# Kernel tuning notes

Hardware: AMD Instinct MI355X
Metric: run time of the kernel (lower is better)

## Reference

```python
import jax, jax.numpy as jnp
import numpy as np

N_NODES = 10000
N_REL = 50
R_AUG = 2 * N_REL + 1  # forward + inverse + self-loop relation
D_EMB = 128
D_H1 = 128
D_H2 = 128
N_EDGES = 320000
N_BATCH = 65536


def setup_inputs() -> dict:
    key = jax.random.key(0)
    ks = jax.random.split(key, 10)
    s = jax.random.randint(ks[0], (N_EDGES,), 0, N_NODES)
    p = jax.random.randint(ks[1], (N_EDGES,), 0, N_REL)
    o = jax.random.randint(ks[2], (N_EDGES,), 0, N_NODES)
    graph = jnp.stack([s, p, o], axis=1)  # [E,3] (subject, relation, object)
    bs = jax.random.randint(ks[3], (N_BATCH,), 0, N_NODES)
    bp = jax.random.randint(ks[4], (N_BATCH,), 0, N_REL)
    bo = jax.random.randint(ks[5], (N_BATCH,), 0, N_NODES)
    batch = jnp.stack([bs, bp, bo], axis=1)  # [B,3] triples to score
    node_embeddings = jax.random.normal(ks[6], (N_NODES, D_EMB), jnp.float32) * 0.02
    W1 = jax.random.normal(ks[7], (R_AUG, D_EMB, D_H1), jnp.float32) * 0.02
    b1 = jnp.zeros((D_H1,), jnp.float32)
    W2 = jax.random.normal(ks[8], (R_AUG, D_H1, D_H2), jnp.float32) * 0.02
    b2 = jnp.zeros((D_H2,), jnp.float32)
    relations = jax.random.normal(ks[9], (N_REL, D_H2), jnp.float32) * 0.02
    return {"graph": graph, "batch": batch, "node_embeddings": node_embeddings,
            "W1": W1, "b1": b1, "W2": W2, "b2": b2, "relations": relations}


def _augment_edges(graph):
    # Add inverse relations (r + N_REL) and self-loops (relation 2*N_REL),
    # matching torch-rgcn's num_relations = nrel*2 + 1 construction.
    s, p, o = graph[:, 0], graph[:, 1], graph[:, 2]
    loop = jnp.arange(N_NODES, dtype=graph.dtype)
    src = jnp.concatenate([s, o, loop])
    rel = jnp.concatenate([p, p + N_REL, jnp.full((N_NODES,), 2 * N_REL, graph.dtype)])
    dst = jnp.concatenate([o, s, loop])
    return src, rel, dst


def _rgcn_layer(x, src, rel, dst, W, b):
    # Per-(relation, target-node) row normalization 1/c_{i,r}, then
    # h_i = sum_r W_r^T * sum_{j in N_r(i)} x_j / c_{i,r} + b
    seg = rel * N_NODES + dst  # segment id over stacked (R*N) adjacency rows
    deg = jax.ops.segment_sum(jnp.ones_like(seg, dtype=x.dtype), seg,
                              num_segments=R_AUG * N_NODES)
    norm = 1.0 / jnp.maximum(deg, 1.0)
    msg = x[src] * norm[seg][:, None]                      # [Etot, d_in]
    agg = jax.ops.segment_sum(msg, seg, num_segments=R_AUG * N_NODES)
    agg = agg.reshape(R_AUG, N_NODES, -1)                  # [R, N, d_in]
    return jnp.einsum('rnd,rdo->no', agg, W) + b           # [N, d_out]


def reference(graph, batch, node_embeddings, W1, b1, W2, b2, relations):
    src, rel, dst = _augment_edges(graph)
    x = _rgcn_layer(node_embeddings, src, rel, dst, W1, b1)
    x = jax.nn.relu(x)
    x = _rgcn_layer(x, src, rel, dst, W2, b2)
    # DistMult scoring: gather s/p/o embeddings, elementwise multiply, reduce.
    s_e = x[batch[:, 0]]
    p_e = relations[batch[:, 1]]
    o_e = x[batch[:, 2]]
    return (s_e * p_e * o_e).sum(axis=1)  # [B]
```

## Files before the change

### kernel.cpp

```cpp
#include <hip/hip_runtime.h>

#define N_NODES 10000
#define N_RELS  50
#define R_AUG   101
#define D       128
#define N_EDGES 320000
#define E_AUG   650000
#define N_BATCH 65536

#define NBINS   N_NODES
#define NSB     ((NBINS + 255) / 256)
#define NP      (R_AUG * N_NODES)
#define NPB4    ((NP + 1023) / 1024)
#define BSPAN   512
#define GEMM_NBLK (101 + (E_AUG + BSPAN - 1) / BSPAN)
#define SCAT_BLOCKS ((E_AUG + 255) / 256)

#define HIST_BLOCKS  2540
#define TW_BLOCKS    808
#define PREPX_BLOCKS 1250

typedef short bf16x8 __attribute__((ext_vector_type(8)));
typedef float f32x4  __attribute__((ext_vector_type(4)));

__device__ __forceinline__ unsigned short f2bf(float f) {
    union { float f; unsigned int u; } v; v.f = f;
    unsigned int r = (v.u + 0x7FFFu + ((v.u >> 16) & 1u)) >> 16;
    return (unsigned short)r;
}
__device__ __forceinline__ float bf2f(unsigned short h) {
    union { unsigned int u; float f; } v; v.u = ((unsigned int)h) << 16;
    return v.f;
}
__device__ __forceinline__ float u2f(unsigned int u) {
    union { unsigned int u; float f; } v; v.u = u; return v.f;
}
__device__ __forceinline__ unsigned int f2u(float f) {
    union { float f; unsigned int u; } v; v.f = f; return v.u;
}

__device__ __forceinline__ void decode_edge(const int* __restrict__ g, int e,
                                            int& src, int& rel, int& dst) {
    if (e < N_EDGES)            { src = g[3*e];     rel = g[3*e+1];          dst = g[3*e+2]; }
    else if (e < 2*N_EDGES)     { int b = e - N_EDGES;
                                  src = g[3*b+2];   rel = g[3*b+1] + N_RELS; dst = g[3*b];   }
    else                        { int n = e - 2*N_EDGES; src = n; dst = n; rel = 2*N_RELS;   }
}

__device__ __forceinline__ int pair_rel(int r) {
    return (r < N_RELS) ? r + N_RELS : (r < 2 * N_RELS ? r - N_RELS : r);
}


__global__ __launch_bounds__(256) void prep_all(const float* __restrict__ x,
                                                unsigned short* __restrict__ xb,
                                                const float* __restrict__ W1,
                                                const float* __restrict__ W2,
                                                unsigned short* __restrict__ W1t,
                                                unsigned short* __restrict__ W2t,
                                                const int* __restrict__ g,
                                                int* __restrict__ deg) {
    __shared__ float tile[64][65];
    int b = blockIdx.x, t = threadIdx.x;
    if (b < HIST_BLOCKS) {
        int e = b * 256 + t;
        if (e < E_AUG) {
            int src, rel, dst;
            decode_edge(g, e, src, rel, dst);
            atomicAdd(&deg[rel * N_NODES + dst], 1);
        }
    } else if (b < HIST_BLOCKS + TW_BLOCKS) {
        int q = b - HIST_BLOCKS;
        int d0 = (q & 1) * 64, o0 = ((q >> 1) & 1) * 64;
        int z = q >> 2;
        const float* W = (z < R_AUG) ? W1 : W2;
        unsigned short* Wt = (z < R_AUG) ? W1t : W2t;
        int r = (z < R_AUG) ? z : (z - R_AUG);
        int tx = t & 63, ty = t >> 6;
        #pragma unroll
        for (int i = ty; i < 64; i += 4)
            tile[i][tx] = W[((size_t)r * D + (d0 + i)) * D + (o0 + tx)];
        __syncthreads();
        #pragma unroll
        for (int i = ty; i < 64; i += 4)
            Wt[((size_t)r * D + (o0 + i)) * D + (d0 + tx)] = f2bf(tile[tx][i]);
    } else {
        int i = (b - HIST_BLOCKS - TW_BLOCKS) * 1024 + t * 4;
        float4 xv = *(const float4*)(x + i);
        ushort4 o;
        o.x = f2bf(xv.x); o.y = f2bf(xv.y); o.z = f2bf(xv.z); o.w = f2bf(xv.w);
        *(ushort4*)(xb + i) = o;
    }
}


__global__ __launch_bounds__(256) void scan_a(const int* __restrict__ deg,
                                              int* __restrict__ offs,
                                              int* __restrict__ part,
                                              int* __restrict__ S,
                                              int* __restrict__ ppart) {
    __shared__ int wsum[4];
    int t = threadIdx.x, lane = t & 63, w = t >> 6;
    int b = blockIdx.x;
    if (b < NSB) {
        int i = b * 256 + t;
        int v = 0;
        if (i < NBINS) {
            for (int r = 0; r < R_AUG; r++) v += deg[r * N_NODES + i];
        }
        int incl = v;
        #pragma unroll
        for (int off = 1; off < 64; off <<= 1) {
            int u = __shfl_up(incl, off, 64);
            if (lane >= off) incl += u;
        }
        if (lane == 63) wsum[w] = incl;
        __syncthreads();
        int woff = 0;
        for (int k = 0; k < w; k++) woff += wsum[k];
        if (i < NBINS) offs[i] = woff + incl - v;
        if (t == 255) part[b] = woff + incl;
    } else {
        int pb = b - NSB;
        int i0 = pb * 1024 + t * 4;
        int4 f = {0, 0, 0, 0};
        if (i0 < NP) {
            int r = i0 / N_NODES;
            int xx = i0 - r * N_NODES;
            const int* dp = deg + pair_rel(r) * N_NODES + xx;
            if (i0 + 3 < NP) {
                int4 d = *(const int4*)dp;
                f.x = d.x > 0; f.y = d.y > 0; f.z = d.z > 0; f.w = d.w > 0;
            } else {
                f.x = dp[0] > 0;
                if (i0 + 1 < NP) f.y = dp[1] > 0;
                if (i0 + 2 < NP) f.z = dp[2] > 0;
            }
        }
        int e1 = f.x, e2 = f.x + f.y, e3 = e2 + f.z, v = e3 + f.w;
        int incl = v;
        #pragma unroll
        for (int off = 1; off < 64; off <<= 1) {
            int u = __shfl_up(incl, off, 64);
            if (lane >= off) incl += u;
        }
        if (lane == 63) wsum[w] = incl;
        __syncthreads();
        int woff = 0;
        for (int k = 0; k < w; k++) woff += wsum[k];
        int texcl = woff + incl - v;
        if (i0 + 3 < NP) {
            int4 o = {texcl, texcl + e1, texcl + e2, texcl + e3};
            *(int4*)(S + i0) = o;
        } else if (i0 < NP) {
            S[i0] = texcl;
            if (i0 + 1 < NP) S[i0 + 1] = texcl + e1;
            if (i0 + 2 < NP) S[i0 + 2] = texcl + e2;
        }
        if (t == 255) ppart[pb] = woff + incl;
    }
}


__global__ __launch_bounds__(256) void scan_b(int* __restrict__ part,
                                              int* __restrict__ ppart,
                                              int* __restrict__ S) {
    __shared__ int wsum[4];
    int t = threadIdx.x, lane = t & 63, w = t >> 6;
    if (blockIdx.x == 0) {
        int v = (t < NSB) ? part[t] : 0;
        int incl = v;
        #pragma unroll
        for (int off = 1; off < 64; off <<= 1) {
            int u = __shfl_up(incl, off, 64);
            if (lane >= off) incl += u;
        }
        if (lane == 63) wsum[w] = incl;
        __syncthreads();
        int woff = 0;
        for (int k = 0; k < w; k++) woff += wsum[k];
        if (t < NSB) part[t] = woff + incl - v;
    } else {
        int carry = 0;
        for (int base = 0; base < NPB4; base += 256) {
            int i = base + t;
            int v = (i < NPB4) ? ppart[i] : 0;
            int incl = v;
            #pragma unroll
            for (int off = 1; off < 64; off <<= 1) {
                int u = __shfl_up(incl, off, 64);
                if (lane >= off) incl += u;
            }
            if (lane == 63) wsum[w] = incl;
            __syncthreads();
            int woff = 0;
            for (int k = 0; k < w; k++) woff += wsum[k];
            if (i < NPB4) ppart[i] = carry + woff + incl - v;
            carry += wsum[0] + wsum[1] + wsum[2] + wsum[3];
            __syncthreads();
        }
        if (t == 0) S[NP] = carry;
    }
}


__global__ __launch_bounds__(256) void scan_c(int* __restrict__ offs,
                                              const int* __restrict__ part,
                                              int* __restrict__ cursor,
                                              const int* __restrict__ deg,
                                              int* __restrict__ S,
                                              const int* __restrict__ ppart,
                                              int* __restrict__ pair_src) {
    int b = blockIdx.x, t = threadIdx.x;
    if (b < NSB) {
        int i = b * 256 + t;
        if (i < NBINS) {
            int v = offs[i] + part[i >> 8];
            offs[i] = v;
            cursor[i] = v;
        }
        if (i == 0) offs[NBINS] = E_AUG;
    } else {
        int pb = b - NSB;
        int i0 = pb * 1024 + t * 4;
        if (i0 >= NP) return;
        int pp = ppart[pb];
        int r = i0 / N_NODES;
        int xx = i0 - r * N_NODES;
        const int* dp = deg + pair_rel(r) * N_NODES + xx;
        if (i0 + 3 < NP) {
            int4 sv = *(int4*)(S + i0);
            sv.x += pp; sv.y += pp; sv.z += pp; sv.w += pp;
            *(int4*)(S + i0) = sv;
            int4 d = *(const int4*)dp;
            if (d.x > 0) pair_src[sv.x] = xx;
            if (d.y > 0) pair_src[sv.y] = xx + 1;
            if (d.z > 0) pair_src[sv.z] = xx + 2;
            if (d.w > 0) pair_src[sv.w] = xx + 3;
        } else {
            for (int k = 0; k < 4; k++) {
                int i = i0 + k;
                if (i >= NP) break;
                int s = S[i] + pp;
                S[i] = s;
                if (dp[k] > 0) pair_src[s] = xx + k;
            }
        }
    }
}


__global__ __launch_bounds__(256) void scatter_blk(const int* __restrict__ g,
                                                   const int* __restrict__ deg,
                                                   const int* __restrict__ S,
                                                   int* __restrict__ cursor,
                                                   uint2* __restrict__ sorted,
                                                   int* __restrict__ rowbase,
                                                   int* __restrict__ rowcnt,
                                                   int* __restrict__ blkoffs) {
    int b = blockIdx.x, t = threadIdx.x;
    if (b == 0) {
        __shared__ int wsum[4];
        int lane = t & 63, w = t >> 6;
        int nb = 0;
        if (t < R_AUG) {
            int base = S[t * N_NODES];
            int nxt  = S[(t + 1) * N_NODES];
            rowbase[t] = base;
            rowcnt[t]  = nxt - base;
            nb = (nxt - base + BSPAN - 1) / BSPAN;
        }
        int incl = nb;
        #pragma unroll
        for (int off = 1; off < 64; off <<= 1) {
            int u = __shfl_up(incl, off, 64);
            if (lane >= off) incl += u;
        }
        if (lane == 63) wsum[w] = incl;
        __syncthreads();
        int woff = 0;
        for (int k = 0; k < w; k++) woff += wsum[k];
        if (t < R_AUG) blkoffs[t] = woff + incl - nb;
        if (t == R_AUG) blkoffs[R_AUG] = woff + incl;
        return;
    }
    int e = (b - 1) * 256 + t;
    if (e >= E_AUG) return;
    int src, rel, dst;
    decode_edge(g, e, src, rel, dst);
    int pos = atomicAdd(&cursor[dst], 1);
    int dg = deg[rel * N_NODES + dst];
    uint2 rec;
    rec.x = (unsigned)S[rel * N_NODES + src];
    rec.y = f2u(1.0f / (float)dg);
    sorted[pos] = rec;
}


__global__ __launch_bounds__(256, 4) void gemm_compact(const unsigned short* __restrict__ xb,
                                                       const unsigned short* __restrict__ Wt,
                                                       const int* __restrict__ pair_src,
                                                       const int* __restrict__ rowbase,
                                                       const int* __restrict__ rowcnt,
                                                       const int* __restrict__ blkoffs,
                                                       unsigned short* __restrict__ Zc) {
    int b = blockIdx.x;
    if (b >= blkoffs[R_AUG]) return;
    int lo = 0, hi = R_AUG;
    while (hi - lo > 1) {
        int mid = (lo + hi) >> 1;
        if (blkoffs[mid] <= b) lo = mid; else hi = mid;
    }
    int r = lo;
    int lb = b - blkoffs[r];
    int rbase = rowbase[r] + lb * BSPAN;
    int nrows = rowcnt[r] - lb * BSPAN; if (nrows > BSPAN) nrows = BSPAN;

    int t = threadIdx.x, wave = t >> 6, lane = t & 63;
    int lr = lane & 15, lq = lane >> 4;
    int no = (wave & 1) * 64;
    int tp = wave >> 1;
    const unsigned short* Wr = Wt + (size_t)r * D * D;

    int srcs[16];
    #pragma unroll
    for (int i = 0; i < 16; i++) {
        int row = (tp + 2 * i) * 16 + lr;
        srcs[i] = pair_src[rbase + (row < nrows ? row : 0)];
    }

    int prow = ((lr >> 2) << 3) + (lr & 3);
    bf16x8 w0[4], w1[4], w2[4], w3[4];
    #pragma unroll
    for (int ks = 0; ks < 4; ks++) {
        size_t kb = ks * 32 + lq * 8;
        w0[ks] = *(const bf16x8*)(Wr + (size_t)(no + prow) * D + kb);
        w1[ks] = *(const bf16x8*)(Wr + (size_t)(no + prow + 4) * D + kb);
        w2[ks] = *(const bf16x8*)(Wr + (size_t)(no + 32 + prow) * D + kb);
        w3[ks] = *(const bf16x8*)(Wr + (size_t)(no + 32 + prow + 4) * D + kb);
    }

    bf16x8 a[4];
    {
        const unsigned short* x0 = xb + (size_t)srcs[0] * D + lq * 8;
        #pragma unroll
        for (int ks = 0; ks < 4; ks++) a[ks] = *(const bf16x8*)(x0 + ks * 32);
    }

    #pragma unroll
    for (int i = 0; i < 16; i++) {
        int tile = tp + 2 * i;
        if (tile * 16 >= nrows) break;

        bf16x8 an[4];
        {
            int ni = (i < 15) ? i + 1 : 15;
            const unsigned short* xn = xb + (size_t)srcs[ni] * D + lq * 8;
            #pragma unroll
            for (int ks = 0; ks < 4; ks++) an[ks] = *(const bf16x8*)(xn + ks * 32);
        }

        f32x4 c0 = {}, c1 = {}, c2 = {}, c3 = {};
        #pragma unroll
        for (int ks = 0; ks < 4; ks++) {
            c0 = __builtin_amdgcn_mfma_f32_16x16x32_bf16(w0[ks], a[ks], c0, 0, 0, 0);
            c1 = __builtin_amdgcn_mfma_f32_16x16x32_bf16(w1[ks], a[ks], c1, 0, 0, 0);
            c2 = __builtin_amdgcn_mfma_f32_16x16x32_bf16(w2[ks], a[ks], c2, 0, 0, 0);
            c3 = __builtin_amdgcn_mfma_f32_16x16x32_bf16(w3[ks], a[ks], c3, 0, 0, 0);
        }
        int row = tile * 16 + lr;
        if (row < nrows) {
            unsigned short* zrow = Zc + ((size_t)(rbase + row) << 7);
            uint4 p0, p1;
            p0.x = (unsigned)f2bf(c0[0]) | ((unsigned)f2bf(c0[1]) << 16);
            p0.y = (unsigned)f2bf(c0[2]) | ((unsigned)f2bf(c0[3]) << 16);
            p0.z = (unsigned)f2bf(c1[0]) | ((unsigned)f2bf(c1[1]) << 16);
            p0.w = (unsigned)f2bf(c1[2]) | ((unsigned)f2bf(c1[3]) << 16);
            p1.x = (unsigned)f2bf(c2[0]) | ((unsigned)f2bf(c2[1]) << 16);
            p1.y = (unsigned)f2bf(c2[2]) | ((unsigned)f2bf(c2[3]) << 16);
            p1.z = (unsigned)f2bf(c3[0]) | ((unsigned)f2bf(c3[1]) << 16);
            p1.w = (unsigned)f2bf(c3[2]) | ((unsigned)f2bf(c3[3]) << 16);
            *(uint4*)(zrow + no + lq * 8) = p0;
            *(uint4*)(zrow + no + 32 + lq * 8) = p1;
        }
        #pragma unroll
        for (int ks = 0; ks < 4; ks++) a[ks] = an[ks];
    }
}


__global__ __launch_bounds__(256) void agg_pass(const uint2* __restrict__ sorted,
                                                const int* __restrict__ offs,
                                                const unsigned short* __restrict__ Zc,
                                                const float* __restrict__ bias,
                                                float* __restrict__ hf,
                                                unsigned short* __restrict__ hb,
                                                int dorelu) {
    int w = threadIdx.x >> 6, lane = threadIdx.x & 63;
    int dst = blockIdx.x * 4 + w;
    if (dst >= N_NODES) return;
    int e0 = offs[dst], e1 = offs[dst + 1];
    int g = lane >> 3, s = lane & 7;
    float acc[16] = {};

    for (int base = e0; base < e1; base += 64) {
        int n = e1 - base; if (n > 64) n = 64;
        uint2 rec = {0u, 0u};
        if (lane < n) rec = sorted[base + lane];
        int iters = (n + 7) >> 3;
        #pragma unroll 2
        for (int j = 0; j < iters; j++) {
            int ej = j * 8 + g;
            int ec = (ej < n) ? ej : (n - 1);
            unsigned zi = (unsigned)__shfl((int)rec.x, ec, 64);
            unsigned nb = (unsigned)__shfl((int)rec.y, ec, 64);
            float nrm = (ej < n) ? u2f(nb) : 0.0f;
            const unsigned short* zp = Zc + ((size_t)zi << 7) + s * 16;
            uint4 z0 = *(const uint4*)zp;
            uint4 z1 = *(const uint4*)(zp + 8);
            acc[0]  += nrm * bf2f((unsigned short)(z0.x & 0xFFFFu));
            acc[1]  += nrm * bf2f((unsigned short)(z0.x >> 16));
            acc[2]  += nrm * bf2f((unsigned short)(z0.y & 0xFFFFu));
            acc[3]  += nrm * bf2f((unsigned short)(z0.y >> 16));
            acc[4]  += nrm * bf2f((unsigned short)(z0.z & 0xFFFFu));
            acc[5]  += nrm * bf2f((unsigned short)(z0.z >> 16));
            acc[6]  += nrm * bf2f((unsigned short)(z0.w & 0xFFFFu));
            acc[7]  += nrm * bf2f((unsigned short)(z0.w >> 16));
            acc[8]  += nrm * bf2f((unsigned short)(z1.x & 0xFFFFu));
            acc[9]  += nrm * bf2f((unsigned short)(z1.x >> 16));
            acc[10] += nrm * bf2f((unsigned short)(z1.y & 0xFFFFu));
            acc[11] += nrm * bf2f((unsigned short)(z1.y >> 16));
            acc[12] += nrm * bf2f((unsigned short)(z1.z & 0xFFFFu));
            acc[13] += nrm * bf2f((unsigned short)(z1.z >> 16));
            acc[14] += nrm * bf2f((unsigned short)(z1.w & 0xFFFFu));
            acc[15] += nrm * bf2f((unsigned short)(z1.w >> 16));
        }
    }
    #pragma unroll
    for (int k = 0; k < 16; k++) {
        acc[k] += __shfl_down(acc[k], 8, 64);
        acc[k] += __shfl_down(acc[k], 16, 64);
        acc[k] += __shfl_down(acc[k], 32, 64);
    }
    if (g == 0) {
        const float* bp = bias + s * 16;
        float vv[16];
        #pragma unroll
        for (int k = 0; k < 16; k++) vv[k] = bp[k] + acc[k];
        if (dorelu) {
            unsigned short* hp = hb + ((size_t)dst << 7) + s * 16;
            uint4 p0, p1;
            p0.x = (unsigned)f2bf(fmaxf(vv[0], 0.0f))  | ((unsigned)f2bf(fmaxf(vv[1], 0.0f))  << 16);
            p0.y = (unsigned)f2bf(fmaxf(vv[2], 0.0f))  | ((unsigned)f2bf(fmaxf(vv[3], 0.0f))  << 16);
            p0.z = (unsigned)f2bf(fmaxf(vv[4], 0.0f))  | ((unsigned)f2bf(fmaxf(vv[5], 0.0f))  << 16);
            p0.w = (unsigned)f2bf(fmaxf(vv[6], 0.0f))  | ((unsigned)f2bf(fmaxf(vv[7], 0.0f))  << 16);
            p1.x = (unsigned)f2bf(fmaxf(vv[8], 0.0f))  | ((unsigned)f2bf(fmaxf(vv[9], 0.0f))  << 16);
            p1.y = (unsigned)f2bf(fmaxf(vv[10], 0.0f)) | ((unsigned)f2bf(fmaxf(vv[11], 0.0f)) << 16);
            p1.z = (unsigned)f2bf(fmaxf(vv[12], 0.0f)) | ((unsigned)f2bf(fmaxf(vv[13], 0.0f)) << 16);
            p1.w = (unsigned)f2bf(fmaxf(vv[14], 0.0f)) | ((unsigned)f2bf(fmaxf(vv[15], 0.0f)) << 16);
            *(uint4*)hp = p0;
            *(uint4*)(hp + 8) = p1;
        } else {
            float* hp = hf + ((size_t)dst << 7) + s * 16;
            #pragma unroll
            for (int q = 0; q < 4; q++) {
                float4 o = {vv[q * 4], vv[q * 4 + 1], vv[q * 4 + 2], vv[q * 4 + 3]};
                *(float4*)(hp + q * 4) = o;
            }
        }
    }
}


__global__ __launch_bounds__(256) void score_kernel(const int* __restrict__ batch,
                                                    const float* __restrict__ h2,
                                                    const float* __restrict__ rels,
                                                    float* __restrict__ out) {
    int t = threadIdx.x;
    int wv = t >> 6, q = (t & 63) >> 4, sl = t & 15;
    int i = blockIdx.x * 16 + wv * 4 + q;
    int bs = batch[3*i], bp = batch[3*i+1], bo = batch[3*i+2];
    const float* sp = h2   + (size_t)bs * D + sl * 8;
    const float* pp = rels + (size_t)bp * D + sl * 8;
    const float* op = h2   + (size_t)bo * D + sl * 8;
    float4 s0 = *(const float4*)sp,      s1 = *(const float4*)(sp + 4);
    float4 p0 = *(const float4*)pp,      p1 = *(const float4*)(pp + 4);
    float4 o0 = *(const float4*)op,      o1 = *(const float4*)(op + 4);
    float v = s0.x * p0.x * o0.x + s0.y * p0.y * o0.y + s0.z * p0.z * o0.z + s0.w * p0.w * o0.w
            + s1.x * p1.x * o1.x + s1.y * p1.y * o1.y + s1.z * p1.z * o1.z + s1.w * p1.w * o1.w;
    #pragma unroll
    for (int off = 8; off > 0; off >>= 1) v += __shfl_down(v, off, 16);
    if (sl == 0) out[i] = v;
}


extern "C" void kernel_launch(void* const* d_in, const int* in_sizes, int n_in,
                              void* d_out, int out_size, void* d_ws, size_t ws_size,
                              hipStream_t stream) {
    const int*   graph = (const int*)  d_in[0];
    const int*   batch = (const int*)  d_in[1];
    const float* emb   = (const float*)d_in[2];
    const float* W1    = (const float*)d_in[3];
    const float* b1    = (const float*)d_in[4];
    const float* W2    = (const float*)d_in[5];
    const float* b2    = (const float*)d_in[6];
    const float* rels  = (const float*)d_in[7];
    float* out = (float*)d_out;

    char* base = (char*)d_ws;
    size_t off = 0;
    auto take = [&](size_t bytes) -> char* {
        char* q = base + off;
        off += (bytes + 255) & ~(size_t)255;
        return q;
    };
    int*            deg     = (int*)           take((size_t)NP * 4);
    int*            S       = (int*)           take((size_t)(NP + 1) * 4);
    int*            pair_src= (int*)           take((size_t)E_AUG * 4);
    int*            ppart   = (int*)           take((size_t)NPB4 * 4);
    int*            rowbase = (int*)           take((size_t)(R_AUG + 1) * 4);
    int*            rowcnt  = (int*)           take((size_t)(R_AUG + 1) * 4);
    int*            blkoffs = (int*)           take((size_t)(R_AUG + 2) * 4);
    unsigned short* xb      = (unsigned short*)take((size_t)N_NODES * D * 2);
    float*          h2      = (float*)         take((size_t)N_NODES * D * 4);
    unsigned short* h1b     = (unsigned short*)take((size_t)N_NODES * D * 2);
    unsigned short* W1t     = (unsigned short*)take((size_t)R_AUG * D * D * 2);
    unsigned short* W2t     = (unsigned short*)take((size_t)R_AUG * D * D * 2);
    int*            offs    = (int*)           take((size_t)(NBINS + 1) * 4);
    int*            cursor  = (int*)           take((size_t)NBINS * 4);
    int*            part    = (int*)           take((size_t)NSB * 4);
    uint2*          sorted  = (uint2*)         take((size_t)E_AUG * 8);
    unsigned short* Zc      = (unsigned short*)take((size_t)E_AUG * D * 2);

    hipMemsetAsync(deg, 0, (size_t)NP * 4, stream);
    prep_all<<<dim3(HIST_BLOCKS + TW_BLOCKS + PREPX_BLOCKS), 256, 0, stream>>>(
        emb, xb, W1, W2, W1t, W2t, graph, deg);
    scan_a<<<dim3(NSB + NPB4), 256, 0, stream>>>(deg, offs, part, S, ppart);
    scan_b<<<dim3(2), 256, 0, stream>>>(part, ppart, S);
    scan_c<<<dim3(NSB + NPB4), 256, 0, stream>>>(offs, part, cursor, deg, S, ppart, pair_src);
    scatter_blk<<<dim3(1 + SCAT_BLOCKS), 256, 0, stream>>>(
        graph, deg, S, cursor, sorted, rowbase, rowcnt, blkoffs);

    gemm_compact<<<dim3(GEMM_NBLK), 256, 0, stream>>>(xb, W1t, pair_src, rowbase, rowcnt, blkoffs, Zc);
    agg_pass<<<dim3((N_NODES + 3) / 4), 256, 0, stream>>>(sorted, offs, Zc, b1, (float*)0, h1b, 1);
    gemm_compact<<<dim3(GEMM_NBLK), 256, 0, stream>>>(h1b, W2t, pair_src, rowbase, rowcnt, blkoffs, Zc);
    agg_pass<<<dim3((N_NODES + 3) / 4), 256, 0, stream>>>(sorted, offs, Zc, b2, h2, (unsigned short*)0, 0);
    score_kernel<<<dim3(N_BATCH / 16), 256, 0, stream>>>(batch, h2, rels, out);
}
```

Measured before the change: 333.9 us.

## Aggregate-then-transform per relation in fused layer kernel instead of transform-then-aggregate

Replaces the transform-then-aggregate scheme with a per-destination-block kernel. For each relation it first averages neighbour features into shared memory, then applies an MFMA GEMM with that relation's weight and accumulates into a shared fp32 tile. Relations are split across two blocks whose partial results a small finish kernel sums with bias and ReLU. This removes the large per-edge Zc intermediate and the separate scan/scatter bookkeeping. In exchange it does many small GEMMs per block, most with few rows, and leans on the sparsity of relation-destination bins.

```diff
diff --git a/kernel.cpp b/kernel.cpp
--- a/kernel.cpp
+++ b/kernel.cpp
@@ -8,17 +8,19 @@
 #define E_AUG   650000
 #define N_BATCH 65536
 
-#define NBINS   N_NODES
-#define NSB     ((NBINS + 255) / 256)
 #define NP      (R_AUG * N_NODES)
 #define NPB4    ((NP + 1023) / 1024)
-#define BSPAN   512
-#define GEMM_NBLK (101 + (E_AUG + BSPAN - 1) / BSPAN)
 #define SCAT_BLOCKS ((E_AUG + 255) / 256)
 
 #define HIST_BLOCKS  2540
 #define TW_BLOCKS    808
 #define PREPX_BLOCKS 1250
+
+#define DSPAN   32
+#define NDBLK   ((N_NODES + DSPAN - 1) / DSPAN)
+#define RSPLIT  2
+#define FUSE_BLOCKS (NDBLK * RSPLIT)
+#define R_HALF  51
 
 typedef short bf16x8 __attribute__((ext_vector_type(8)));
 typedef float f32x4  __attribute__((ext_vector_type(4)));
@@ -31,12 +33,6 @@
 __device__ __forceinline__ float bf2f(unsigned short h) {
     union { unsigned int u; float f; } v; v.u = ((unsigned int)h) << 16;
     return v.f;
-}
-__device__ __forceinline__ float u2f(unsigned int u) {
-    union { unsigned int u; float f; } v; v.u = u; return v.f;
-}
-__device__ __forceinline__ unsigned int f2u(float f) {
-    union { float f; unsigned int u; } v; v.f = f; return v.u;
 }
 
 __device__ __forceinline__ void decode_edge(const int* __restrict__ g, int e,
@@ -45,10 +41,6 @@
     else if (e < 2*N_EDGES)     { int b = e - N_EDGES;
                                   src = g[3*b+2];   rel = g[3*b+1] + N_RELS; dst = g[3*b];   }
     else                        { int n = e - 2*N_EDGES; src = n; dst = n; rel = 2*N_RELS;   }
-}
-
-__device__ __forceinline__ int pair_rel(int r) {
-    return (r < N_RELS) ? r + N_RELS : (r < 2 * N_RELS ? r - N_RELS : r);
 }
 
 
@@ -67,6 +59,7 @@
         if (e < E_AUG) {
             int src, rel, dst;
             decode_edge(g, e, src, rel, dst);
+            (void)src;
             atomicAdd(&deg[rel * N_NODES + dst], 1);
         }
     } else if (b < HIST_BLOCKS + TW_BLOCKS) {
@@ -95,19 +88,41 @@
 
 
 __global__ __launch_bounds__(256) void scan_a(const int* __restrict__ deg,
-                                              int* __restrict__ offs,
-                                              int* __restrict__ part,
-                                              int* __restrict__ S,
+                                              int* __restrict__ binoff,
                                               int* __restrict__ ppart) {
     __shared__ int wsum[4];
     int t = threadIdx.x, lane = t & 63, w = t >> 6;
-    int b = blockIdx.x;
-    if (b < NSB) {
-        int i = b * 256 + t;
-        int v = 0;
-        if (i < NBINS) {
-            for (int r = 0; r < R_AUG; r++) v += deg[r * N_NODES + i];
-        }
+    int i0 = blockIdx.x * 1024 + t * 4;
+    int4 d = {0, 0, 0, 0};
+    if (i0 < NP) d = *(const int4*)(deg + i0);
+    int e1 = d.x, e2 = e1 + d.y, e3 = e2 + d.z, v = e3 + d.w;
+    int incl = v;
+    #pragma unroll
+    for (int off = 1; off < 64; off <<= 1) {
+        int u = __shfl_up(incl, off, 64);
+        if (lane >= off) incl += u;
+    }
+    if (lane == 63) wsum[w] = incl;
+    __syncthreads();
+    int woff = 0;
+    for (int k = 0; k < w; k++) woff += wsum[k];
+    int texcl = woff + incl - v;
+    if (i0 < NP) {
+        int4 o = {texcl, texcl + e1, texcl + e2, texcl + e3};
+        *(int4*)(binoff + i0) = o;
+    }
+    if (t == 255) ppart[blockIdx.x] = woff + incl;
+}
+
+
+__global__ __launch_bounds__(256) void scan_b(int* __restrict__ ppart,
+                                              int* __restrict__ binoff) {
+    __shared__ int wsum[4];
+    int t = threadIdx.x, lane = t & 63, w = t >> 6;
+    int carry = 0;
+    for (int base = 0; base < NPB4; base += 256) {
+        int i = base + t;
+        int v = (i < NPB4) ? ppart[i] : 0;
         int incl = v;
         #pragma unroll
         for (int off = 1; off < 64; off <<= 1) {
@@ -118,356 +133,239 @@
         __syncthreads();
         int woff = 0;
         for (int k = 0; k < w; k++) woff += wsum[k];
-        if (i < NBINS) offs[i] = woff + incl - v;
-        if (t == 255) part[b] = woff + incl;
-    } else {
-        int pb = b - NSB;
-        int i0 = pb * 1024 + t * 4;
-        int4 f = {0, 0, 0, 0};
-        if (i0 < NP) {
-            int r = i0 / N_NODES;
-            int xx = i0 - r * N_NODES;
-            const int* dp = deg + pair_rel(r) * N_NODES + xx;
-            if (i0 + 3 < NP) {
-                int4 d = *(const int4*)dp;
-                f.x = d.x > 0; f.y = d.y > 0; f.z = d.z > 0; f.w = d.w > 0;
-            } else {
-                f.x = dp[0] > 0;
-                if (i0 + 1 < NP) f.y = dp[1] > 0;
-                if (i0 + 2 < NP) f.z = dp[2] > 0;
-            }
-        }
-        int e1 = f.x, e2 = f.x + f.y, e3 = e2 + f.z, v = e3 + f.w;
-        int incl = v;
-        #pragma unroll
-        for (int off = 1; off < 64; off <<= 1) {
-            int u = __shfl_up(incl, off, 64);
-            if (lane >= off) incl += u;
-        }
-        if (lane == 63) wsum[w] = incl;
+        if (i < NPB4) ppart[i] = carry + woff + incl - v;
+        carry += wsum[0] + wsum[1] + wsum[2] + wsum[3];
         __syncthreads();
-        int woff = 0;
-        for (int k = 0; k < w; k++) woff += wsum[k];
-        int texcl = woff + incl - v;
-        if (i0 + 3 < NP) {
-            int4 o = {texcl, texcl + e1, texcl + e2, texcl + e3};
-            *(int4*)(S + i0) = o;
-        } else if (i0 < NP) {
-            S[i0] = texcl;
-            if (i0 + 1 < NP) S[i0 + 1] = texcl + e1;
-            if (i0 + 2 < NP) S[i0 + 2] = texcl + e2;
-        }
-        if (t == 255) ppart[pb] = woff + incl;
-    }
-}
-
-
-__global__ __launch_bounds__(256) void scan_b(int* __restrict__ part,
-                                              int* __restrict__ ppart,
-                                              int* __restrict__ S) {
-    __shared__ int wsum[4];
-    int t = threadIdx.x, lane = t & 63, w = t >> 6;
-    if (blockIdx.x == 0) {
-        int v = (t < NSB) ? part[t] : 0;
-        int incl = v;
-        #pragma unroll
-        for (int off = 1; off < 64; off <<= 1) {
-            int u = __shfl_up(incl, off, 64);
-            if (lane >= off) incl += u;
-        }
-        if (lane == 63) wsum[w] = incl;
-        __syncthreads();
-        int woff = 0;
-        for (int k = 0; k < w; k++) woff += wsum[k];
-        if (t < NSB) part[t] = woff + incl - v;
-    } else {
-        int carry = 0;
-        for (int base = 0; base < NPB4; base += 256) {
-            int i = base + t;
-            int v = (i < NPB4) ? ppart[i] : 0;
-            int incl = v;
-            #pragma unroll
-            for (int off = 1; off < 64; off <<= 1) {
-                int u = __shfl_up(incl, off, 64);
-                if (lane >= off) incl += u;
-            }
-            if (lane == 63) wsum[w] = incl;
-            __syncthreads();
-            int woff = 0;
-            for (int k = 0; k < w; k++) woff += wsum[k];
-            if (i < NPB4) ppart[i] = carry + woff + incl - v;
-            carry += wsum[0] + wsum[1] + wsum[2] + wsum[3];
-            __syncthreads();
-        }
-        if (t == 0) S[NP] = carry;
-    }
-}
-
-
-__global__ __launch_bounds__(256) void scan_c(int* __restrict__ offs,
-                                              const int* __restrict__ part,
-                                              int* __restrict__ cursor,
-                                              const int* __restrict__ deg,
-                                              int* __restrict__ S,
+    }
+    if (t == 0) binoff[NP] = carry;
+}
+
+
+__global__ __launch_bounds__(256) void scan_c(int* __restrict__ binoff,
                                               const int* __restrict__ ppart,
-                                              int* __restrict__ pair_src) {
-    int b = blockIdx.x, t = threadIdx.x;
-    if (b < NSB) {
-        int i = b * 256 + t;
-        if (i < NBINS) {
-            int v = offs[i] + part[i >> 8];
-            offs[i] = v;
-            cursor[i] = v;
-        }
-        if (i == 0) offs[NBINS] = E_AUG;
-    } else {
-        int pb = b - NSB;
-        int i0 = pb * 1024 + t * 4;
-        if (i0 >= NP) return;
-        int pp = ppart[pb];
-        int r = i0 / N_NODES;
-        int xx = i0 - r * N_NODES;
-        const int* dp = deg + pair_rel(r) * N_NODES + xx;
-        if (i0 + 3 < NP) {
-            int4 sv = *(int4*)(S + i0);
-            sv.x += pp; sv.y += pp; sv.z += pp; sv.w += pp;
-            *(int4*)(S + i0) = sv;
-            int4 d = *(const int4*)dp;
-            if (d.x > 0) pair_src[sv.x] = xx;
-            if (d.y > 0) pair_src[sv.y] = xx + 1;
-            if (d.z > 0) pair_src[sv.z] = xx + 2;
-            if (d.w > 0) pair_src[sv.w] = xx + 3;
-        } else {
-            for (int k = 0; k < 4; k++) {
-                int i = i0 + k;
-                if (i >= NP) break;
-                int s = S[i] + pp;
-                S[i] = s;
-                if (dp[k] > 0) pair_src[s] = xx + k;
-            }
-        }
-    }
-}
-
-
-__global__ __launch_bounds__(256) void scatter_blk(const int* __restrict__ g,
-                                                   const int* __restrict__ deg,
-                                                   const int* __restrict__ S,
-                                                   int* __restrict__ cursor,
-                                                   uint2* __restrict__ sorted,
-                                                   int* __restrict__ rowbase,
-                                                   int* __restrict__ rowcnt,
-                                                   int* __restrict__ blkoffs) {
-    int b = blockIdx.x, t = threadIdx.x;
-    if (b == 0) {
-        __shared__ int wsum[4];
-        int lane = t & 63, w = t >> 6;
-        int nb = 0;
-        if (t < R_AUG) {
-            int base = S[t * N_NODES];
-            int nxt  = S[(t + 1) * N_NODES];
-            rowbase[t] = base;
-            rowcnt[t]  = nxt - base;
-            nb = (nxt - base + BSPAN - 1) / BSPAN;
-        }
-        int incl = nb;
-        #pragma unroll
-        for (int off = 1; off < 64; off <<= 1) {
-            int u = __shfl_up(incl, off, 64);
-            if (lane >= off) incl += u;
-        }
-        if (lane == 63) wsum[w] = incl;
-        __syncthreads();
-        int woff = 0;
-        for (int k = 0; k < w; k++) woff += wsum[k];
-        if (t < R_AUG) blkoffs[t] = woff + incl - nb;
-        if (t == R_AUG) blkoffs[R_AUG] = woff + incl;
-        return;
-    }
-    int e = (b - 1) * 256 + t;
+                                              int* __restrict__ cursor) {
+    int i0 = blockIdx.x * 1024 + threadIdx.x * 4;
+    if (i0 >= NP) return;
+    int pp = ppart[blockIdx.x];
+    int4 sv = *(int4*)(binoff + i0);
+    sv.x += pp; sv.y += pp; sv.z += pp; sv.w += pp;
+    *(int4*)(binoff + i0) = sv;
+    *(int4*)(cursor + i0) = sv;
+}
+
+
+__global__ __launch_bounds__(256) void scatter_edges(const int* __restrict__ g,
+                                                     int* __restrict__ cursor,
+                                                     unsigned short* __restrict__ esrc) {
+    int e = blockIdx.x * 256 + threadIdx.x;
     if (e >= E_AUG) return;
     int src, rel, dst;
     decode_edge(g, e, src, rel, dst);
-    int pos = atomicAdd(&cursor[dst], 1);
-    int dg = deg[rel * N_NODES + dst];
-    uint2 rec;
-    rec.x = (unsigned)S[rel * N_NODES + src];
-    rec.y = f2u(1.0f / (float)dg);
-    sorted[pos] = rec;
-}
-
-
-__global__ __launch_bounds__(256, 4) void gemm_compact(const unsigned short* __restrict__ xb,
-                                                       const unsigned short* __restrict__ Wt,
-                                                       const int* __restrict__ pair_src,
-                                                       const int* __restrict__ rowbase,
-                                                       const int* __restrict__ rowcnt,
-                                                       const int* __restrict__ blkoffs,
-                                                       unsigned short* __restrict__ Zc) {
+    int pos = atomicAdd(&cursor[rel * N_NODES + dst], 1);
+    esrc[pos] = (unsigned short)src;
+}
+
+
+__global__ __launch_bounds__(256, 2) void fused_layer(const unsigned short* __restrict__ xb,
+                                                      const unsigned short* __restrict__ Wt,
+                                                      const int* __restrict__ binoff,
+                                                      const unsigned short* __restrict__ esrc,
+                                                      float* __restrict__ hpart) {
+    __shared__ __align__(16) char aggbuf[2][DSPAN * D * 2];
+    __shared__ __align__(16) char hblk[DSPAN * D * 4];
+    __shared__ int bbase[2][DSPAN];
+    __shared__ int bpack[2][DSPAN];
+
     int b = blockIdx.x;
-    if (b >= blkoffs[R_AUG]) return;
-    int lo = 0, hi = R_AUG;
-    while (hi - lo > 1) {
-        int mid = (lo + hi) >> 1;
-        if (blkoffs[mid] <= b) lo = mid; else hi = mid;
-    }
-    int r = lo;
-    int lb = b - blkoffs[r];
-    int rbase = rowbase[r] + lb * BSPAN;
-    int nrows = rowcnt[r] - lb * BSPAN; if (nrows > BSPAN) nrows = BSPAN;
-
-    int t = threadIdx.x, wave = t >> 6, lane = t & 63;
+    int half = b & 1, dblk = b >> 1;
+    int dst0 = dblk * DSPAN;
+    int r0 = half ? R_HALF : 0;
+    int r1 = half ? R_AUG : R_HALF;
+
+    int t = threadIdx.x, w = t >> 6, lane = t & 63;
     int lr = lane & 15, lq = lane >> 4;
-    int no = (wave & 1) * 64;
-    int tp = wave >> 1;
-    const unsigned short* Wr = Wt + (size_t)r * D * D;
-
-    int srcs[16];
+
     #pragma unroll
-    for (int i = 0; i < 16; i++) {
-        int row = (tp + 2 * i) * 16 + lr;
-        srcs[i] = pair_src[rbase + (row < nrows ? row : 0)];
-    }
-
+    for (int i = t * 4; i < DSPAN * D; i += 1024) {
+        float4 z = {0.f, 0.f, 0.f, 0.f};
+        *(float4*)(hblk + (size_t)i * 4) = z;
+    }
+
+    auto agg_rel = [&](int r, int B) -> int {
+        int j = lane;
+        int bj = 0;
+        if (j <= DSPAN) {
+            int jj = dst0 + j;
+            if (jj > N_NODES) jj = N_NODES;
+            bj = binoff[r * N_NODES + jj];
+        }
+        int bnext = __shfl_down(bj, 1, 64);
+        int dg = (j < DSPAN) ? (bnext - bj) : 0;
+        unsigned long long m = __ballot(dg > 0);
+        unsigned int mask = (unsigned int)m;
+        int nb = __popc(mask);
+        int cb = __popc(mask & ((j < 32) ? ((1u << j) - 1u) : 0xFFFFFFFFu));
+        if (j < DSPAN && dg > 0 && (cb & 3) == w) {
+            bbase[B][cb] = bj;
+            bpack[B][cb] = (dg << 8) | j;
+        }
+        int mbase[8], mdeg[8];
+        #pragma unroll
+        for (int i = 0; i < 8; i++) {
+            int c = w + 4 * i;
+            if (c < nb) { mbase[i] = bbase[B][c]; mdeg[i] = bpack[B][c] >> 8; }
+            else        { mbase[i] = 0;           mdeg[i] = 0; }
+        }
+        float a0[8], a1[8];
+        #pragma unroll
+        for (int i = 0; i < 8; i++) { a0[i] = 0.f; a1[i] = 0.f; }
+        int k = 0;
+        bool any = (w < nb);
+        while (any) {
+            any = false;
+            int sv[8];
+            unsigned int xv[8];
+            #pragma unroll
+            for (int i = 0; i < 8; i++)
+                if (k < mdeg[i]) sv[i] = esrc[mbase[i] + k];
+            #pragma unroll
+            for (int i = 0; i < 8; i++)
+                if (k < mdeg[i]) xv[i] = *(const unsigned int*)(xb + (size_t)sv[i] * D + lane * 2);
+            #pragma unroll
+            for (int i = 0; i < 8; i++)
+                if (k < mdeg[i]) {
+                    a0[i] += bf2f((unsigned short)(xv[i] & 0xFFFFu));
+                    a1[i] += bf2f((unsigned short)(xv[i] >> 16));
+                    if (k + 1 < mdeg[i]) any = true;
+                }
+            k++;
+        }
+        #pragma unroll
+        for (int i = 0; i < 8; i++)
+            if (mdeg[i] > 0) {
+                float s = 1.0f / (float)mdeg[i];
+                unsigned int pk = (unsigned)f2bf(a0[i] * s) | ((unsigned)f2bf(a1[i] * s) << 16);
+                int c = w + 4 * i;
+                int byteoff = (c * 256 + lane * 4) ^ ((c & 7) << 4);
+                *(unsigned int*)(aggbuf[B] + byteoff) = pk;
+            }
+        return nb;
+    };
+
+    int no = w * 32;
     int prow = ((lr >> 2) << 3) + (lr & 3);
-    bf16x8 w0[4], w1[4], w2[4], w3[4];
-    #pragma unroll
-    for (int ks = 0; ks < 4; ks++) {
-        size_t kb = ks * 32 + lq * 8;
-        w0[ks] = *(const bf16x8*)(Wr + (size_t)(no + prow) * D + kb);
-        w1[ks] = *(const bf16x8*)(Wr + (size_t)(no + prow + 4) * D + kb);
-        w2[ks] = *(const bf16x8*)(Wr + (size_t)(no + 32 + prow) * D + kb);
-        w3[ks] = *(const bf16x8*)(Wr + (size_t)(no + 32 + prow + 4) * D + kb);
-    }
-
-    bf16x8 a[4];
-    {
-        const unsigned short* x0 = xb + (size_t)srcs[0] * D + lq * 8;
-        #pragma unroll
-        for (int ks = 0; ks < 4; ks++) a[ks] = *(const bf16x8*)(x0 + ks * 32);
-    }
-
-    #pragma unroll
-    for (int i = 0; i < 16; i++) {
-        int tile = tp + 2 * i;
-        if (tile * 16 >= nrows) break;
-
-        bf16x8 an[4];
+    auto mfma_rel = [&](int r, int B, int nb) {
+        if (nb <= 0) return;
+        const unsigned short* Wr = Wt + (size_t)r * D * D;
+        bf16x8 w0[4], w1[4];
+        #pragma unroll
+        for (int ks = 0; ks < 4; ks++) {
+            size_t kb = (size_t)ks * 32 + lq * 8;
+            w0[ks] = *(const bf16x8*)(Wr + (size_t)(no + prow) * D + kb);
+            w1[ks] = *(const bf16x8*)(Wr + (size_t)(no + prow + 4) * D + kb);
+        }
         {
-            int ni = (i < 15) ? i + 1 : 15;
-            const unsigned short* xn = xb + (size_t)srcs[ni] * D + lq * 8;
+            f32x4 c0 = {}, c1 = {};
             #pragma unroll
-            for (int ks = 0; ks < 4; ks++) an[ks] = *(const bf16x8*)(xn + ks * 32);
-        }
-
-        f32x4 c0 = {}, c1 = {}, c2 = {}, c3 = {};
-        #pragma unroll
-        for (int ks = 0; ks < 4; ks++) {
-            c0 = __builtin_amdgcn_mfma_f32_16x16x32_bf16(w0[ks], a[ks], c0, 0, 0, 0);
-            c1 = __builtin_amdgcn_mfma_f32_16x16x32_bf16(w1[ks], a[ks], c1, 0, 0, 0);
-            c2 = __builtin_amdgcn_mfma_f32_16x16x32_bf16(w2[ks], a[ks], c2, 0, 0, 0);
-            c3 = __builtin_amdgcn_mfma_f32_16x16x32_bf16(w3[ks], a[ks], c3, 0, 0, 0);
-        }
-        int row = tile * 16 + lr;
-        if (row < nrows) {
-            unsigned short* zrow = Zc + ((size_t)(rbase + row) << 7);
-            uint4 p0, p1;
-            p0.x = (unsigned)f2bf(c0[0]) | ((unsigned)f2bf(c0[1]) << 16);
-            p0.y = (unsigned)f2bf(c0[2]) | ((unsigned)f2bf(c0[3]) << 16);
-            p0.z = (unsigned)f2bf(c1[0]) | ((unsigned)f2bf(c1[1]) << 16);
-            p0.w = (unsigned)f2bf(c1[2]) | ((unsigned)f2bf(c1[3]) << 16);
-            p1.x = (unsigned)f2bf(c2[0]) | ((unsigned)f2bf(c2[1]) << 16);
-            p1.y = (unsigned)f2bf(c2[2]) | ((unsigned)f2bf(c2[3]) << 16);
-            p1.z = (unsigned)f2bf(c3[0]) | ((unsigned)f2bf(c3[1]) << 16);
-            p1.w = (unsigned)f2bf(c3[2]) | ((unsigned)f2bf(c3[3]) << 16);
-            *(uint4*)(zrow + no + lq * 8) = p0;
-            *(uint4*)(zrow + no + 32 + lq * 8) = p1;
-        }
-        #pragma unroll
-        for (int ks = 0; ks < 4; ks++) a[ks] = an[ks];
-    }
-}
-
-
-__global__ __launch_bounds__(256) void agg_pass(const uint2* __restrict__ sorted,
-                                                const int* __restrict__ offs,
-                                                const unsigned short* __restrict__ Zc,
-                                                const float* __restrict__ bias,
-                                                float* __restrict__ hf,
-                                                unsigned short* __restrict__ hb,
-                                                int dorelu) {
-    int w = threadIdx.x >> 6, lane = threadIdx.x & 63;
-    int dst = blockIdx.x * 4 + w;
-    if (dst >= N_NODES) return;
-    int e0 = offs[dst], e1 = offs[dst + 1];
-    int g = lane >> 3, s = lane & 7;
-    float acc[16] = {};
-
-    for (int base = e0; base < e1; base += 64) {
-        int n = e1 - base; if (n > 64) n = 64;
-        uint2 rec = {0u, 0u};
-        if (lane < n) rec = sorted[base + lane];
-        int iters = (n + 7) >> 3;
-        #pragma unroll 2
-        for (int j = 0; j < iters; j++) {
-            int ej = j * 8 + g;
-            int ec = (ej < n) ? ej : (n - 1);
-            unsigned zi = (unsigned)__shfl((int)rec.x, ec, 64);
-            unsigned nb = (unsigned)__shfl((int)rec.y, ec, 64);
-            float nrm = (ej < n) ? u2f(nb) : 0.0f;
-            const unsigned short* zp = Zc + ((size_t)zi << 7) + s * 16;
-            uint4 z0 = *(const uint4*)zp;
-            uint4 z1 = *(const uint4*)(zp + 8);
-            acc[0]  += nrm * bf2f((unsigned short)(z0.x & 0xFFFFu));
-            acc[1]  += nrm * bf2f((unsigned short)(z0.x >> 16));
-            acc[2]  += nrm * bf2f((unsigned short)(z0.y & 0xFFFFu));
-            acc[3]  += nrm * bf2f((unsigned short)(z0.y >> 16));
-            acc[4]  += nrm * bf2f((unsigned short)(z0.z & 0xFFFFu));
-            acc[5]  += nrm * bf2f((unsigned short)(z0.z >> 16));
-            acc[6]  += nrm * bf2f((unsigned short)(z0.w & 0xFFFFu));
-            acc[7]  += nrm * bf2f((unsigned short)(z0.w >> 16));
-            acc[8]  += nrm * bf2f((unsigned short)(z1.x & 0xFFFFu));
-            acc[9]  += nrm * bf2f((unsigned short)(z1.x >> 16));
-            acc[10] += nrm * bf2f((unsigned short)(z1.y & 0xFFFFu));
-            acc[11] += nrm * bf2f((unsigned short)(z1.y >> 16));
-            acc[12] += nrm * bf2f((unsigned short)(z1.z & 0xFFFFu));
-            acc[13] += nrm * bf2f((unsigned short)(z1.z >> 16));
-            acc[14] += nrm * bf2f((unsigned short)(z1.w & 0xFFFFu));
-            acc[15] += nrm * bf2f((unsigned short)(z1.w >> 16));
-        }
-    }
-    #pragma unroll
-    for (int k = 0; k < 16; k++) {
-        acc[k] += __shfl_down(acc[k], 8, 64);
-        acc[k] += __shfl_down(acc[k], 16, 64);
-        acc[k] += __shfl_down(acc[k], 32, 64);
-    }
-    if (g == 0) {
-        const float* bp = bias + s * 16;
-        float vv[16];
-        #pragma unroll
-        for (int k = 0; k < 16; k++) vv[k] = bp[k] + acc[k];
-        if (dorelu) {
-            unsigned short* hp = hb + ((size_t)dst << 7) + s * 16;
-            uint4 p0, p1;
-            p0.x = (unsigned)f2bf(fmaxf(vv[0], 0.0f))  | ((unsigned)f2bf(fmaxf(vv[1], 0.0f))  << 16);
-            p0.y = (unsigned)f2bf(fmaxf(vv[2], 0.0f))  | ((unsigned)f2bf(fmaxf(vv[3], 0.0f))  << 16);
-            p0.z = (unsigned)f2bf(fmaxf(vv[4], 0.0f))  | ((unsigned)f2bf(fmaxf(vv[5], 0.0f))  << 16);
-            p0.w = (unsigned)f2bf(fmaxf(vv[6], 0.0f))  | ((unsigned)f2bf(fmaxf(vv[7], 0.0f))  << 16);
-            p1.x = (unsigned)f2bf(fmaxf(vv[8], 0.0f))  | ((unsigned)f2bf(fmaxf(vv[9], 0.0f))  << 16);
-            p1.y = (unsigned)f2bf(fmaxf(vv[10], 0.0f)) | ((unsigned)f2bf(fmaxf(vv[11], 0.0f)) << 16);
-            p1.z = (unsigned)f2bf(fmaxf(vv[12], 0.0f)) | ((unsigned)f2bf(fmaxf(vv[13], 0.0f)) << 16);
-            p1.w = (unsigned)f2bf(fmaxf(vv[14], 0.0f)) | ((unsigned)f2bf(fmaxf(vv[15], 0.0f)) << 16);
-            *(uint4*)hp = p0;
-            *(uint4*)(hp + 8) = p1;
-        } else {
-            float* hp = hf + ((size_t)dst << 7) + s * 16;
+            for (int ks = 0; ks < 4; ks++) {
+                int byteoff = (lr * 256 + ks * 64 + lq * 16) ^ ((lr & 7) << 4);
+                bf16x8 a = *(const bf16x8*)(aggbuf[B] + byteoff);
+                c0 = __builtin_amdgcn_mfma_f32_16x16x32_bf16(w0[ks], a, c0, 0, 0, 0);
+                c1 = __builtin_amdgcn_mfma_f32_16x16x32_bf16(w1[ks], a, c1, 0, 0, 0);
+            }
+            if (lr < nb) {
+                int dloc = bpack[B][lr] & 63;
+                int cbyte = (no + lq * 8) * 4;
+                char* hp0 = hblk + (((dloc * 512) + cbyte) ^ ((dloc & 7) << 5));
+                char* hp1 = hblk + (((dloc * 512) + cbyte + 16) ^ ((dloc & 7) << 5));
+                float4 h0 = *(float4*)hp0;
+                h0.x += c0[0]; h0.y += c0[1]; h0.z += c0[2]; h0.w += c0[3];
+                *(float4*)hp0 = h0;
+                float4 h1 = *(float4*)hp1;
+                h1.x += c1[0]; h1.y += c1[1]; h1.z += c1[2]; h1.w += c1[3];
+                *(float4*)hp1 = h1;
+            }
+        }
+        if (nb > 16) {
+            f32x4 c2 = {}, c3 = {};
+            int rrow = 16 + lr;
             #pragma unroll
-            for (int q = 0; q < 4; q++) {
-                float4 o = {vv[q * 4], vv[q * 4 + 1], vv[q * 4 + 2], vv[q * 4 + 3]};
-                *(float4*)(hp + q * 4) = o;
+            for (int ks = 0; ks < 4; ks++) {
+                int byteoff = (rrow * 256 + ks * 64 + lq * 16) ^ ((rrow & 7) << 4);
+                bf16x8 a = *(const bf16x8*)(aggbuf[B] + byteoff);
+                c2 = __builtin_amdgcn_mfma_f32_16x16x32_bf16(w0[ks], a, c2, 0, 0, 0);
+                c3 = __builtin_amdgcn_mfma_f32_16x16x32_bf16(w1[ks], a, c3, 0, 0, 0);
             }
-        }
+            if (rrow < nb) {
+                int dloc = bpack[B][rrow] & 63;
+                int cbyte = (no + lq * 8) * 4;
+                char* hp0 = hblk + (((dloc * 512) + cbyte) ^ ((dloc & 7) << 5));
+                char* hp1 = hblk + (((dloc * 512) + cbyte + 16) ^ ((dloc & 7) << 5));
+                float4 h0 = *(float4*)hp0;
+                h0.x += c2[0]; h0.y += c2[1]; h0.z += c2[2]; h0.w += c2[3];
+                *(float4*)hp0 = h0;
+                float4 h1 = *(float4*)hp1;
+                h1.x += c3[0]; h1.y += c3[1]; h1.z += c3[2]; h1.w += c3[3];
+                *(float4*)hp1 = h1;
+            }
+        }
+    };
+
+    int nbC = agg_rel(r0, 0);
+    __syncthreads();
+    int cur = 0;
+    for (int r = r0; r < r1; r++) {
+        int nbN = 0;
+        if (r + 1 < r1) nbN = agg_rel(r + 1, cur ^ 1);
+        mfma_rel(r, cur, nbC);
+        __syncthreads();
+        nbC = nbN;
+        cur ^= 1;
+    }
+
+    int row = t >> 3, c0b = (t & 7) * 16;
+    int dst = dst0 + row;
+    if (dst < N_NODES) {
+        float* outp = hpart + (size_t)half * N_NODES * D + (size_t)dst * D;
+        #pragma unroll
+        for (int q = 0; q < 4; q++) {
+            int cb = c0b + q * 4;
+            float4 v = *(float4*)(hblk + (((row * 512) + cb * 4) ^ ((row & 7) << 5)));
+            *(float4*)(outp + cb) = v;
+        }
+    }
+}
+
+
+__global__ __launch_bounds__(256) void finish(const float* __restrict__ hpart,
+                                              const float* __restrict__ bias,
+                                              float* __restrict__ hf,
+                                              unsigned short* __restrict__ hb,
+                                              int dorelu) {
+    int i0 = (blockIdx.x * 256 + threadIdx.x) * 8;
+    int c0 = i0 & 127;
+    const float* p0 = hpart + i0;
+    const float* p1 = hpart + (size_t)N_NODES * D + i0;
+    float4 x0 = *(const float4*)p0,        x1 = *(const float4*)(p0 + 4);
+    float4 y0 = *(const float4*)p1,        y1 = *(const float4*)(p1 + 4);
+    float4 b0 = *(const float4*)(bias + c0), b1 = *(const float4*)(bias + c0 + 4);
+    float v[8];
+    v[0] = x0.x + y0.x + b0.x; v[1] = x0.y + y0.y + b0.y;
+    v[2] = x0.z + y0.z + b0.z; v[3] = x0.w + y0.w + b0.w;
+    v[4] = x1.x + y1.x + b1.x; v[5] = x1.y + y1.y + b1.y;
+    v[6] = x1.z + y1.z + b1.z; v[7] = x1.w + y1.w + b1.w;
+    if (dorelu) {
+        uint4 p;
+        p.x = (unsigned)f2bf(fmaxf(v[0], 0.f)) | ((unsigned)f2bf(fmaxf(v[1], 0.f)) << 16);
+        p.y = (unsigned)f2bf(fmaxf(v[2], 0.f)) | ((unsigned)f2bf(fmaxf(v[3], 0.f)) << 16);
+        p.z = (unsigned)f2bf(fmaxf(v[4], 0.f)) | ((unsigned)f2bf(fmaxf(v[5], 0.f)) << 16);
+        p.w = (unsigned)f2bf(fmaxf(v[6], 0.f)) | ((unsigned)f2bf(fmaxf(v[7], 0.f)) << 16);
+        *(uint4*)(hb + i0) = p;
+    } else {
+        float4 o0 = {v[0], v[1], v[2], v[3]};
+        float4 o1 = {v[4], v[5], v[6], v[7]};
+        *(float4*)(hf + i0) = o0;
+        *(float4*)(hf + i0 + 4) = o1;
     }
 }
 
@@ -515,35 +413,28 @@
         return q;
     };
     int*            deg     = (int*)           take((size_t)NP * 4);
-    int*            S       = (int*)           take((size_t)(NP + 1) * 4);
-    int*            pair_src= (int*)           take((size_t)E_AUG * 4);
+    int*            binoff  = (int*)           take((size_t)(NP + 1) * 4);
+    int*            cursor  = (int*)           take((size_t)NP * 4);
     int*            ppart   = (int*)           take((size_t)NPB4 * 4);
-    int*            rowbase = (int*)           take((size_t)(R_AUG + 1) * 4);
-    int*            rowcnt  = (int*)           take((size_t)(R_AUG + 1) * 4);
-    int*            blkoffs = (int*)           take((size_t)(R_AUG + 2) * 4);
+    unsigned short* esrc    = (unsigned short*)take((size_t)E_AUG * 2);
     unsigned short* xb      = (unsigned short*)take((size_t)N_NODES * D * 2);
+    unsigned short* h1b     = (unsigned short*)take((size_t)N_NODES * D * 2);
     float*          h2      = (float*)         take((size_t)N_NODES * D * 4);
-    unsigned short* h1b     = (unsigned short*)take((size_t)N_NODES * D * 2);
     unsigned short* W1t     = (unsigned short*)take((size_t)R_AUG * D * D * 2);
     unsigned short* W2t     = (unsigned short*)take((size_t)R_AUG * D * D * 2);
-    int*            offs    = (int*)           take((size_t)(NBINS + 1) * 4);
-    int*            cursor  = (int*)           take((size_t)NBINS * 4);
-    int*            part    = (int*)           take((size_t)NSB * 4);
-    uint2*          sorted  = (uint2*)         take((size_t)E_AUG * 8);
-    unsigned short* Zc      = (unsigned short*)take((size_t)E_AUG * D * 2);
+    float*          hpart   = (float*)         take((size_t)RSPLIT * N_NODES * D * 4);
 
     hipMemsetAsync(deg, 0, (size_t)NP * 4, stream);
     prep_all<<<dim3(HIST_BLOCKS + TW_BLOCKS + PREPX_BLOCKS), 256, 0, stream>>>(
         emb, xb, W1, W2, W1t, W2t, graph, deg);
-    scan_a<<<dim3(NSB + NPB4), 256, 0, stream>>>(deg, offs, part, S, ppart);
-    scan_b<<<dim3(2), 256, 0, stream>>>(part, ppart, S);
-    scan_c<<<dim3(NSB + NPB4), 256, 0, stream>>>(offs, part, cursor, deg, S, ppart, pair_src);
-    scatter_blk<<<dim3(1 + SCAT_BLOCKS), 256, 0, stream>>>(
-        graph, deg, S, cursor, sorted, rowbase, rowcnt, blkoffs);
-
-    gemm_compact<<<dim3(GEMM_NBLK), 256, 0, stream>>>(xb, W1t, pair_src, rowbase, rowcnt, blkoffs, Zc);
-    agg_pass<<<dim3((N_NODES + 3) / 4), 256, 0, stream>>>(sorted, offs, Zc, b1, (float*)0, h1b, 1);
-    gemm_compact<<<dim3(GEMM_NBLK), 256, 0, stream>>>(h1b, W2t, pair_src, rowbase, rowcnt, blkoffs, Zc);
-    agg_pass<<<dim3((N_NODES + 3) / 4), 256, 0, stream>>>(sorted, offs, Zc, b2, h2, (unsigned short*)0, 0);
+    scan_a<<<dim3(NPB4), 256, 0, stream>>>(deg, binoff, ppart);
+    scan_b<<<dim3(1), 256, 0, stream>>>(ppart, binoff);
+    scan_c<<<dim3(NPB4), 256, 0, stream>>>(binoff, ppart, cursor);
+    scatter_edges<<<dim3(SCAT_BLOCKS), 256, 0, stream>>>(graph, cursor, esrc);
+
+    fused_layer<<<dim3(FUSE_BLOCKS), 256, 0, stream>>>(xb, W1t, binoff, esrc, hpart);
+    finish<<<dim3(625), 256, 0, stream>>>(hpart, b1, (float*)0, h1b, 1);
+    fused_layer<<<dim3(FUSE_BLOCKS), 256, 0, stream>>>(h1b, W2t, binoff, esrc, hpart);
+    finish<<<dim3(625), 256, 0, stream>>>(hpart, b2, h2, (unsigned short*)0, 0);
     score_kernel<<<dim3(N_BATCH / 16), 256, 0, stream>>>(batch, h2, rels, out);
 }
```

New measurement: 668.2 us. +100.1%, slower.
